# Kernel tuning notes

Measured on AMD Instinct MI355X. Metric: run time of the kernel, lower is better.

## Reference

```python
import jax, jax.numpy as jnp
import numpy as np

B, C, F_IN, F_OUT = 2048, 63, 250, 250
NEG_SLOPE = 0.2
N = B * C  # flattened node count


def _build_edge_index():
    # fixed fully-connected (no self) graph over the FIRST 63 nodes only
    src = np.array([i for i in range(C) for j in range(C) if i != j], dtype=np.int32)
    dst = np.array([j for i in range(C) for j in range(C) if i != j], dtype=np.int32)
    # PyG GATConv add_self_loops=True: self loop for every node (num_nodes = N)
    loops = np.arange(N, dtype=np.int32)
    src = np.concatenate([src, loops])
    dst = np.concatenate([dst, loops])
    return jnp.asarray(np.stack([src, dst]))  # [2, E]


def setup_inputs() -> dict:
    key = jax.random.key(0)
    kx, kw, ks, kd = jax.random.split(key, 4)
    x = jax.random.normal(kx, (B, 1, C, F_IN), dtype=jnp.float32)
    # GATConv params (heads=1): lin weight, att_src, att_dst, bias
    W = jax.random.normal(kw, (F_IN, F_OUT), dtype=jnp.float32) / np.sqrt(F_IN)
    att_src = jax.random.normal(ks, (F_OUT,), dtype=jnp.float32) / np.sqrt(F_OUT)
    att_dst = jax.random.normal(kd, (F_OUT,), dtype=jnp.float32) / np.sqrt(F_OUT)
    bias = jnp.zeros((F_OUT,), dtype=jnp.float32)
    return {"x": x, "W": W, "att_src": att_src, "att_dst": att_dst,
            "bias": bias, "edge_index": _build_edge_index()}


def reference(x, W, att_src, att_dst, bias, edge_index):
    b, _, c, f = x.shape
    n = b * c
    h = x.reshape(n, f) @ W                      # [N, F_OUT]
    a_src = h @ att_src                          # [N]
    a_dst = h @ att_dst                          # [N]
    src, dst = edge_index[0], edge_index[1]
    e = jax.nn.leaky_relu(a_src[src] + a_dst[dst], NEG_SLOPE)  # [E]
    # segment softmax over incoming edges of each dst node (stable)
    m = jax.ops.segment_max(e, dst, num_segments=n)
    ex = jnp.exp(e - m[dst])
    denom = jax.ops.segment_sum(ex, dst, num_segments=n)
    alpha = ex / denom[dst]                      # [E]
    out = jax.ops.segment_sum(alpha[:, None] * h[src], dst, num_segments=n)
    out = out + bias
    return out.reshape(b, 1, c, -1)              # [B,1,63,F_OUT]
```

## Files before the change

kernel.cpp:

```cpp
#include <hip/hip_runtime.h>
#include <cstdint>
#include <cstddef>

#define M_TOTAL 129024
#define KDIM    250
#define NDIM    250
#define BM      32
#define NBLK    4032
#define TILE_F  (BM*KDIM)

typedef float  f32x4  __attribute__((ext_vector_type(4)));
typedef float  f32x2  __attribute__((ext_vector_type(2)));
typedef __bf16 bf16x8 __attribute__((ext_vector_type(8)));

static __device__ __forceinline__ unsigned short f2bf(float f) {
  unsigned u = __float_as_uint(f);
  u += 0x7fffu + ((u >> 16) & 1u);
  return (unsigned short)(u >> 16);
}

static __device__ __forceinline__ float wsum(float v) {
#pragma unroll
  for (int o = 32; o > 0; o >>= 1) v += __shfl_xor(v, o, 64);
  return v;
}
static __device__ __forceinline__ float wmaxr(float v) {
#pragma unroll
  for (int o = 32; o > 0; o >>= 1) v = fmaxf(v, __shfl_xor(v, o, 64));
  return v;
}

static __device__ __forceinline__ void gll16(const float* g, float* l) {
  __builtin_amdgcn_global_load_lds(
      (const __attribute__((address_space(1))) void*)g,
      (__attribute__((address_space(3))) void*)l, 16, 0, 0);
}
static __device__ __forceinline__ void gll4(const float* g, float* l) {
  __builtin_amdgcn_global_load_lds(
      (const __attribute__((address_space(1))) void*)g,
      (__attribute__((address_space(3))) void*)l, 4, 0, 0);
}

__global__ void wcvt_kernel(const float* __restrict__ W, unsigned short* __restrict__ WTf) {
  const int f     = blockIdx.x * 256 + threadIdx.x;
  const int lane  = f & 63;
  const int kk    = (f >> 6) & 7;
  const int ntile = f >> 9;
  const int n     = ntile * 16 + (lane & 15);
  const int k0    = kk * 32 + (lane >> 4) * 8;
  unsigned u[4];
#pragma unroll
  for (int p = 0; p < 4; ++p) {
    const int ka = k0 + 2 * p, kb = k0 + 2 * p + 1;
    unsigned short a = (n < NDIM && ka < KDIM) ? f2bf(W[(size_t)ka * NDIM + n]) : 0;
    unsigned short b = (n < NDIM && kb < KDIM) ? f2bf(W[(size_t)kb * NDIM + n]) : 0;
    u[p] = (unsigned)a | ((unsigned)b << 16);
  }
  *reinterpret_cast<uint4*>(WTf + (size_t)f * 8) = make_uint4(u[0], u[1], u[2], u[3]);
}

__global__ __launch_bounds__(256, 4) void gemm_kernel(
    const float* __restrict__ X, const unsigned short* __restrict__ WTf,
    const float* __restrict__ bias, float* __restrict__ out,
    float* __restrict__ h63) {
  __shared__ __attribute__((aligned(16))) float lX[TILE_F + 8];

  const int tid  = threadIdx.x;
  const int lane = tid & 63;
  const int w    = tid >> 6;
  const int r16  = lane & 15;
  const int quad = lane >> 4;

  if (tid < 8) lX[TILE_F + tid] = 0.f;

  {
    const float* gb = X + (size_t)blockIdx.x * TILE_F;
    if (w < 3) {
#pragma unroll
      for (int c = 0; c < 8; ++c) {
        const int ch = w * 8 + c;
        gll16(gb + ch * 256 + lane * 4, lX + ch * 256);
      }
    } else {
#pragma unroll
      for (int c = 0; c < 7; ++c) {
        const int ch = 24 + c;
        gll16(gb + ch * 256 + lane * 4, lX + ch * 256);
      }
      gll4(gb + 7936 + lane, lX + 7936);
    }
  }

  float bv[4][4];
#pragma unroll
  for (int ft = 0; ft < 4; ++ft)
#pragma unroll
    for (int i = 0; i < 4; ++i) {
      const int c = w * 64 + ft * 16 + quad * 4 + i;
      bv[ft][i] = (c < NDIM) ? bias[c] : 0.f;
    }

  __syncthreads();

  f32x4 acc[4][2];
#pragma unroll
  for (int ft = 0; ft < 4; ++ft)
#pragma unroll
    for (int nt = 0; nt < 2; ++nt) acc[ft][nt] = f32x4{0.f, 0.f, 0.f, 0.f};

  const unsigned short* wp = WTf + (size_t)(((w * 4) * 8) * 64 + lane) * 8;
  const size_t ft_str = (size_t)8 * 64 * 8;
  const size_t kk_str = (size_t)64 * 8;

  bf16x8 wc[4], wn[4];
#pragma unroll
  for (int ft = 0; ft < 4; ++ft)
    wc[ft] = *reinterpret_cast<const bf16x8*>(wp + ft * ft_str);

#pragma unroll 1
  for (int kk = 0; kk < 8; ++kk) {
    if (kk < 7) {
#pragma unroll
      for (int ft = 0; ft < 4; ++ft)
        wn[ft] = *reinterpret_cast<const bf16x8*>(wp + ft * ft_str + (kk + 1) * kk_str);
    }
    bf16x8 xf[2];
#pragma unroll
    for (int nt = 0; nt < 2; ++nt) {
      const float* p = lX + (size_t)(nt * 16 + r16) * KDIM + kk * 32 + quad * 8;
      const f32x2 a = *reinterpret_cast<const f32x2*>(p);
      const f32x2 b = *reinterpret_cast<const f32x2*>(p + 2);
      const f32x2 c = *reinterpret_cast<const f32x2*>(p + 4);
      const f32x2 d = *reinterpret_cast<const f32x2*>(p + 6);
      bf16x8 v;
      v[0] = (__bf16)a.x; v[1] = (__bf16)a.y;
      v[2] = (__bf16)b.x; v[3] = (__bf16)b.y;
      v[4] = (__bf16)c.x; v[5] = (__bf16)c.y;
      v[6] = (__bf16)d.x; v[7] = (__bf16)d.y;
      xf[nt] = v;
    }
#pragma unroll
    for (int ft = 0; ft < 4; ++ft)
#pragma unroll
      for (int nt = 0; nt < 2; ++nt)
        acc[ft][nt] = __builtin_amdgcn_mfma_f32_16x16x32_bf16(
            wc[ft], xf[nt], acc[ft][nt], 0, 0, 0);
#pragma unroll
    for (int ft = 0; ft < 4; ++ft) wc[ft] = wn[ft];
  }

  const int rbase = blockIdx.x * BM;
  if (blockIdx.x < 2) {
#pragma unroll
    for (int ft = 0; ft < 4; ++ft) {
      const int c0 = w * 64 + ft * 16 + quad * 4;
#pragma unroll
      for (int nt = 0; nt < 2; ++nt) {
        const int row = rbase + nt * 16 + r16;
        if (row < 63) {
          const f32x4 a = acc[ft][nt];
#pragma unroll
          for (int i = 0; i < 4; ++i)
            if (c0 + i < NDIM) h63[(size_t)row * NDIM + c0 + i] = a[i];
        }
      }
    }
  }

  __syncthreads();

#pragma unroll
  for (int ft = 0; ft < 4; ++ft) {
    const int c0 = w * 64 + ft * 16 + quad * 4;
#pragma unroll
    for (int nt = 0; nt < 2; ++nt) {
      const int row = nt * 16 + r16;
      float* o = lX + (size_t)row * KDIM + c0;
      const f32x4 a = acc[ft][nt];
      if (c0 + 3 < NDIM) {
        *reinterpret_cast<f32x2*>(o)     = f32x2{a.x + bv[ft][0], a.y + bv[ft][1]};
        *reinterpret_cast<f32x2*>(o + 2) = f32x2{a.z + bv[ft][2], a.w + bv[ft][3]};
      } else if (c0 + 1 < NDIM) {
        *reinterpret_cast<f32x2*>(o) = f32x2{a.x + bv[ft][0], a.y + bv[ft][1]};
      }
    }
  }

  __syncthreads();

  float* ob = out + (size_t)blockIdx.x * TILE_F;
#pragma unroll
  for (int c = 0; c < 8; ++c) {
    const int flat = c * 1024 + tid * 4;
    if (c < 7 || tid < 208) {
      const f32x4 v = *reinterpret_cast<const f32x4*>(lX + flat);
      __builtin_nontemporal_store(v, reinterpret_cast<f32x4*>(ob + flat));
    }
  }
}

__global__ void att_kernel(const float* __restrict__ h, const float* __restrict__ att_src,
                           const float* __restrict__ att_dst, const float* __restrict__ bias,
                           float* __restrict__ out) {
  const int d = blockIdx.x;
  const int tid = threadIdx.x;
  const int lane = tid & 63;
  const int wid = tid >> 6;

  __shared__ float s_asrc[64];
  __shared__ float s_adst;
  __shared__ float s_alpha[64];

  for (int s = wid; s < 63; s += 4) {
    float sum = 0.f;
    for (int f = lane; f < NDIM; f += 64) sum += h[s * NDIM + f] * att_src[f];
    sum = wsum(sum);
    if (lane == 0) s_asrc[s] = sum;
  }
  if (wid == 0) {
    float sum = 0.f;
    for (int f = lane; f < NDIM; f += 64) sum += h[d * NDIM + f] * att_dst[f];
    sum = wsum(sum);
    if (lane == 0) s_adst = sum;
  }
  __syncthreads();

  if (wid == 0) {
    float e = -__builtin_inff();
    if (lane < 63) {
      float x = s_asrc[lane] + s_adst;
      e = (x > 0.f) ? x : 0.2f * x;
    }
    const float m = wmaxr(e);
    const float p = (lane < 63) ? expf(e - m) : 0.f;
    const float den = wsum(p);
    s_alpha[lane] = p / den;
  }
  __syncthreads();

  const int f = tid;
  if (f < NDIM) {
    float o = bias[f];
    for (int s = 0; s < 63; ++s) o += s_alpha[s] * h[s * NDIM + f];
    out[(size_t)d * NDIM + f] = o;
  }
}

extern "C" void kernel_launch(void* const* d_in, const int* in_sizes, int n_in,
                              void* d_out, int out_size, void* d_ws, size_t ws_size,
                              hipStream_t stream) {
  const float* X       = (const float*)d_in[0];
  const float* W       = (const float*)d_in[1];
  const float* att_src = (const float*)d_in[2];
  const float* att_dst = (const float*)d_in[3];
  const float* bias    = (const float*)d_in[4];
  float* out = (float*)d_out;

  unsigned short* WTf = (unsigned short*)d_ws;
  float* h63 = (float*)((char*)d_ws + 131072);

  wcvt_kernel<<<32, 256, 0, stream>>>(W, WTf);
  gemm_kernel<<<NBLK, 256, 0, stream>>>(X, WTf, bias, out, h63);
  att_kernel<<<63, 256, 0, stream>>>(h63, att_src, att_dst, bias, out);
}
```

Before: 275.2 us.

## Process two row tiles per GEMM block with staged loads overlapping compute

```diff
diff --git a/kernel.cpp b/kernel.cpp
--- a/kernel.cpp
+++ b/kernel.cpp
@@ -6,7 +6,8 @@
 #define KDIM    250
 #define NDIM    250
 #define BM      32
-#define NBLK    4032
+#define TPB     2
+#define NBLK    2016
 #define TILE_F  (BM*KDIM)
 
 typedef float  f32x4  __attribute__((ext_vector_type(4)));
@@ -59,11 +60,11 @@
   *reinterpret_cast<uint4*>(WTf + (size_t)f * 8) = make_uint4(u[0], u[1], u[2], u[3]);
 }
 
-__global__ __launch_bounds__(256, 4) void gemm_kernel(
+__global__ __launch_bounds__(256, 2) void gemm_kernel(
     const float* __restrict__ X, const unsigned short* __restrict__ WTf,
     const float* __restrict__ bias, float* __restrict__ out,
     float* __restrict__ h63) {
-  __shared__ __attribute__((aligned(16))) float lX[TILE_F + 8];
+  __shared__ __attribute__((aligned(16))) float lX[16016];
 
   const int tid  = threadIdx.x;
   const int lane = tid & 63;
@@ -71,25 +72,7 @@
   const int r16  = lane & 15;
   const int quad = lane >> 4;
 
-  if (tid < 8) lX[TILE_F + tid] = 0.f;
-
-  {
-    const float* gb = X + (size_t)blockIdx.x * TILE_F;
-    if (w < 3) {
-#pragma unroll
-      for (int c = 0; c < 8; ++c) {
-        const int ch = w * 8 + c;
-        gll16(gb + ch * 256 + lane * 4, lX + ch * 256);
-      }
-    } else {
-#pragma unroll
-      for (int c = 0; c < 7; ++c) {
-        const int ch = 24 + c;
-        gll16(gb + ch * 256 + lane * 4, lX + ch * 256);
-      }
-      gll4(gb + 7936 + lane, lX + 7936);
-    }
-  }
+  if (tid < 8) { lX[8000 + tid] = 0.f; lX[16008 + tid] = 0.f; }
 
   float bv[4][4];
 #pragma unroll
@@ -100,69 +83,101 @@
       bv[ft][i] = (c < NDIM) ? bias[c] : 0.f;
     }
 
-  __syncthreads();
-
-  f32x4 acc[4][2];
-#pragma unroll
-  for (int ft = 0; ft < 4; ++ft)
-#pragma unroll
-    for (int nt = 0; nt < 2; ++nt) acc[ft][nt] = f32x4{0.f, 0.f, 0.f, 0.f};
-
-  const unsigned short* wp = WTf + (size_t)(((w * 4) * 8) * 64 + lane) * 8;
+  auto stage = [&](float* lb, int g) {
+    const float* gb = X + (size_t)g * TILE_F;
+    if (w < 3) {
+#pragma unroll
+      for (int c = 0; c < 8; ++c) {
+        const int ch = w * 8 + c;
+        gll16(gb + ch * 256 + lane * 4, lb + ch * 256);
+      }
+    } else {
+#pragma unroll
+      for (int c = 0; c < 7; ++c) {
+        const int ch = 24 + c;
+        gll16(gb + ch * 256 + lane * 4, lb + ch * 256);
+      }
+      gll4(gb + 7936 + lane, lb + 7936);
+    }
+  };
+
+  const int t0 = blockIdx.x * TPB;
+  stage(&lX[0], t0);
+  stage(&lX[8008], t0 + 1);
+
+  const unsigned short* wpb = WTf + (size_t)(((w * 4) * 8) * 64 + lane) * 8;
   const size_t ft_str = (size_t)8 * 64 * 8;
   const size_t kk_str = (size_t)64 * 8;
-
-  bf16x8 wc[4], wn[4];
-#pragma unroll
-  for (int ft = 0; ft < 4; ++ft)
-    wc[ft] = *reinterpret_cast<const bf16x8*>(wp + ft * ft_str);
-
+  auto compute = [&](const float* Bp, f32x4 (&acc)[4][2]) {
+#pragma unroll
+    for (int ft = 0; ft < 4; ++ft)
+#pragma unroll
+      for (int nt = 0; nt < 2; ++nt) acc[ft][nt] = f32x4{0.f, 0.f, 0.f, 0.f};
+    bf16x8 wc[4], wn[4];
+#pragma unroll
+    for (int ft = 0; ft < 4; ++ft)
+      wc[ft] = *reinterpret_cast<const bf16x8*>(wpb + ft * ft_str);
 #pragma unroll 1
-  for (int kk = 0; kk < 8; ++kk) {
-    if (kk < 7) {
+    for (int kk = 0; kk < 8; ++kk) {
+      if (kk < 7) {
+#pragma unroll
+        for (int ft = 0; ft < 4; ++ft)
+          wn[ft] = *reinterpret_cast<const bf16x8*>(wpb + ft * ft_str + (kk + 1) * kk_str);
+      }
+      bf16x8 xf[2];
+#pragma unroll
+      for (int nt = 0; nt < 2; ++nt) {
+        const float* p = Bp + (size_t)(nt * 16 + r16) * KDIM + kk * 32 + quad * 8;
+        const f32x2 a = *reinterpret_cast<const f32x2*>(p);
+        const f32x2 b = *reinterpret_cast<const f32x2*>(p + 2);
+        const f32x2 c = *reinterpret_cast<const f32x2*>(p + 4);
+        const f32x2 d = *reinterpret_cast<const f32x2*>(p + 6);
+        bf16x8 v;
+        v[0] = (__bf16)a.x; v[1] = (__bf16)a.y;
+        v[2] = (__bf16)b.x; v[3] = (__bf16)b.y;
+        v[4] = (__bf16)c.x; v[5] = (__bf16)c.y;
+        v[6] = (__bf16)d.x; v[7] = (__bf16)d.y;
+        xf[nt] = v;
+      }
 #pragma unroll
       for (int ft = 0; ft < 4; ++ft)
-        wn[ft] = *reinterpret_cast<const bf16x8*>(wp + ft * ft_str + (kk + 1) * kk_str);
-    }
-    bf16x8 xf[2];
-#pragma unroll
-    for (int nt = 0; nt < 2; ++nt) {
-      const float* p = lX + (size_t)(nt * 16 + r16) * KDIM + kk * 32 + quad * 8;
-      const f32x2 a = *reinterpret_cast<const f32x2*>(p);
-      const f32x2 b = *reinterpret_cast<const f32x2*>(p + 2);
-      const f32x2 c = *reinterpret_cast<const f32x2*>(p + 4);
-      const f32x2 d = *reinterpret_cast<const f32x2*>(p + 6);
-      bf16x8 v;
-      v[0] = (__bf16)a.x; v[1] = (__bf16)a.y;
-      v[2] = (__bf16)b.x; v[3] = (__bf16)b.y;
-      v[4] = (__bf16)c.x; v[5] = (__bf16)c.y;
-      v[6] = (__bf16)d.x; v[7] = (__bf16)d.y;
-      xf[nt] = v;
-    }
-#pragma unroll
-    for (int ft = 0; ft < 4; ++ft)
-#pragma unroll
-      for (int nt = 0; nt < 2; ++nt)
-        acc[ft][nt] = __builtin_amdgcn_mfma_f32_16x16x32_bf16(
-            wc[ft], xf[nt], acc[ft][nt], 0, 0, 0);
-#pragma unroll
-    for (int ft = 0; ft < 4; ++ft) wc[ft] = wn[ft];
-  }
-
-  const int rbase = blockIdx.x * BM;
-  if (blockIdx.x < 2) {
+#pragma unroll
+        for (int nt = 0; nt < 2; ++nt)
+          acc[ft][nt] = __builtin_amdgcn_mfma_f32_16x16x32_bf16(
+              wc[ft], xf[nt], acc[ft][nt], 0, 0, 0);
+#pragma unroll
+      for (int ft = 0; ft < 4; ++ft) wc[ft] = wn[ft];
+    }
+  };
+
+  asm volatile("s_waitcnt vmcnt(8) lgkmcnt(0)" ::: "memory");
+  __builtin_amdgcn_s_barrier();
+
+  f32x4 accA[4][2];
+  compute(&lX[0], accA);
+
+  asm volatile("s_waitcnt vmcnt(0)" ::: "memory");
+  __builtin_amdgcn_s_barrier();
+
+  f32x4 accB[4][2];
+  compute(&lX[8008], accB);
+
+  if (blockIdx.x == 0) {
 #pragma unroll
     for (int ft = 0; ft < 4; ++ft) {
       const int c0 = w * 64 + ft * 16 + quad * 4;
 #pragma unroll
       for (int nt = 0; nt < 2; ++nt) {
-        const int row = rbase + nt * 16 + r16;
-        if (row < 63) {
-          const f32x4 a = acc[ft][nt];
-#pragma unroll
-          for (int i = 0; i < 4; ++i)
-            if (c0 + i < NDIM) h63[(size_t)row * NDIM + c0 + i] = a[i];
-        }
+        const int rowA = nt * 16 + r16;
+        const int rowB = 32 + nt * 16 + r16;
+        const f32x4 a = accA[ft][nt];
+        const f32x4 b = accB[ft][nt];
+#pragma unroll
+        for (int i = 0; i < 4; ++i)
+          if (c0 + i < NDIM) {
+            h63[(size_t)rowA * NDIM + c0 + i] = a[i];
+            if (rowB < 63) h63[(size_t)rowB * NDIM + c0 + i] = b[i];
+          }
       }
     }
   }
@@ -175,24 +190,29 @@
 #pragma unroll
     for (int nt = 0; nt < 2; ++nt) {
       const int row = nt * 16 + r16;
-      float* o = lX + (size_t)row * KDIM + c0;
-      const f32x4 a = acc[ft][nt];
+      float* oA = lX + (size_t)row * KDIM + c0;
+      float* oB = lX + 8000 + (size_t)row * KDIM + c0;
+      const f32x4 a = accA[ft][nt];
+      const f32x4 b = accB[ft][nt];
       if (c0 + 3 < NDIM) {
-        *reinterpret_cast<f32x2*>(o)     = f32x2{a.x + bv[ft][0], a.y + bv[ft][1]};
-        *reinterpret_cast<f32x2*>(o + 2) = f32x2{a.z + bv[ft][2], a.w + bv[ft][3]};
+        *reinterpret_cast<f32x2*>(oA)     = f32x2{a.x + bv[ft][0], a.y + bv[ft][1]};
+        *reinterpret_cast<f32x2*>(oA + 2) = f32x2{a.z + bv[ft][2], a.w + bv[ft][3]};
+        *reinterpret_cast<f32x2*>(oB)     = f32x2{b.x + bv[ft][0], b.y + bv[ft][1]};
+        *reinterpret_cast<f32x2*>(oB + 2) = f32x2{b.z + bv[ft][2], b.w + bv[ft][3]};
       } else if (c0 + 1 < NDIM) {
-        *reinterpret_cast<f32x2*>(o) = f32x2{a.x + bv[ft][0], a.y + bv[ft][1]};
-      }
-    }
-  }
-
-  __syncthreads();
-
-  float* ob = out + (size_t)blockIdx.x * TILE_F;
-#pragma unroll
-  for (int c = 0; c < 8; ++c) {
+        *reinterpret_cast<f32x2*>(oA) = f32x2{a.x + bv[ft][0], a.y + bv[ft][1]};
+        *reinterpret_cast<f32x2*>(oB) = f32x2{b.x + bv[ft][0], b.y + bv[ft][1]};
+      }
+    }
+  }
+
+  __syncthreads();
+
+  float* ob = out + (size_t)blockIdx.x * (TPB * TILE_F);
+#pragma unroll
+  for (int c = 0; c < 16; ++c) {
     const int flat = c * 1024 + tid * 4;
-    if (c < 7 || tid < 208) {
+    if (c < 15 || tid < 160) {
       const f32x4 v = *reinterpret_cast<const f32x4*>(lX + flat);
       __builtin_nontemporal_store(v, reinterpret_cast<f32x4*>(ob + flat));
     }
```

After: 274.3 us. About the same (-0.3%).
